# Optimization experiments

Hardware: AMD Instinct MI355X
Metric: run time of the kernel (lower is better)

The kernel has to match this reference:

```python
import jax, jax.numpy as jnp
import numpy as np

KSIZE = 16  # sliding window length (module ksize)


def setup_inputs() -> dict:
    key = jax.random.key(0)
    k0, k1, k2, k3, k4 = jax.random.split(key, 5)
    B, L, D, H = 16, 1024, 256, 256
    s = 1.0 / np.sqrt(H)  # torch RNN default init: U(-1/sqrt(H), 1/sqrt(H))
    x = jax.random.normal(k0, (B, L, D), dtype=jnp.float32)
    W_ih = jax.random.uniform(k1, (3 * H, D), jnp.float32, -s, s)  # [r|z|n] rows
    W_hh = jax.random.uniform(k2, (3 * H, H), jnp.float32, -s, s)
    b_ih = jax.random.uniform(k3, (3 * H,), jnp.float32, -s, s)
    b_hh = jax.random.uniform(k4, (3 * H,), jnp.float32, -s, s)
    return {"x": x, "W_ih": W_ih, "W_hh": W_hh, "b_ih": b_ih, "b_hh": b_hh}


def reference(x, W_ih, W_hh, b_ih, b_hh):
    # LocalRNN forward: for each position l, run a GRU over the window
    # x[l-K+1 : l+1] (zero left-padded) and emit the final hidden state.
    # Instead of materializing the [B, L, K, D] windowed copy (torch get_K),
    # we scan over the K window steps, slicing the padded input each step.
    B, L, D = x.shape
    H = W_hh.shape[1]
    K = KSIZE
    xpad = jnp.concatenate([jnp.zeros((B, K - 1, D), x.dtype), x], axis=1)  # [B, L+K-1, D]

    def step(h, t):
        xt = jax.lax.dynamic_slice_in_dim(xpad, t, L, axis=1)  # [B, L, D] = window step t for every position
        gi = jnp.einsum('bld,gd->blg', xt, W_ih) + b_ih          # [B, L, 3H]
        gh = jnp.einsum('blh,gh->blg', h, W_hh) + b_hh           # [B, L, 3H]
        i_r, i_z, i_n = jnp.split(gi, 3, axis=-1)
        h_r, h_z, h_n = jnp.split(gh, 3, axis=-1)
        r = jax.nn.sigmoid(i_r + h_r)
        z = jax.nn.sigmoid(i_z + h_z)
        n = jnp.tanh(i_n + r * h_n)
        h_new = (1.0 - z) * n + z * h  # torch GRU update
        return h_new, None

    h0 = jnp.zeros((B, L, H), x.dtype)
    h_final, _ = jax.lax.scan(step, h0, jnp.arange(K))
    return h_final  # [B, L, H] == h.view(batch, l, output_dim)
```

## Files before the change

### kernel.cpp

```cpp
#include <hip/hip_runtime.h>
#include <hip/hip_bf16.h>
#include <cstdint>


#define B_  16
#define L_  1024
#define D_  256
#define H_  256
#define K_  16
#define MT  32
#define NROW 47
#define HS  264
#define GRS 258
#define GNS 264
#define L2E 1.44269504f
#define NWR 196608

typedef __attribute__((ext_vector_type(8))) short  bf16x8;
typedef __attribute__((ext_vector_type(4))) float  floatx4;
typedef unsigned short ush;

#if __has_builtin(__builtin_amdgcn_exp2f)
#define fexp2(x) __builtin_amdgcn_exp2f(x)
#else
#define fexp2(x) exp2f(x)
#endif

__device__ __forceinline__ float bf2f(ush u) {
    union { unsigned int i; float f; } v; v.i = ((unsigned int)u) << 16; return v.f;
}
__device__ __forceinline__ ush f2bf(float f) {
    union { float f; unsigned int i; } v; v.f = f;
    unsigned int x = v.i;
    return (ush)((x + 0x7FFFu + ((x >> 16) & 1u)) >> 16);
}
__device__ __forceinline__ unsigned int pk2(float a, float b) {
    union { __hip_bfloat162 v; unsigned int u; } c;
    c.v = __float22bfloat162_rn(make_float2(a, b));
    return c.u;
}
__device__ __forceinline__ float rcpf(float x) { return __builtin_amdgcn_rcpf(x); }

#define NCHUNK 24576
__global__ __launch_bounds__(256) void wprep(const float* __restrict__ Wih,
                                             const float* __restrict__ Whh,
                                             ush* __restrict__ Wir,
                                             ush* __restrict__ Wr) {
    int idx = blockIdx.x * 256 + threadIdx.x;
    const float* src = (idx < NCHUNK) ? Whh : Wih;
    ush* dst         = (idx < NCHUNK) ? Wr  : Wir;
    int c = (idx < NCHUNK) ? idx : idx - NCHUNK;
    int srow = c >> 5, ch = c & 31;
    int gate = srow >> 8, rr = srow & 255;
    int w    = rr >> 5;
    int sloc = (rr >> 4) & 1;
    int l16  = rr & 15;
    int ks   = ch >> 2;
    int quad = ch & 3;
    int lane = quad * 16 + l16;
    int e0 = (((w * 6 + gate * 2 + sloc) * 8 + ks) << 9) + lane * 8;
    float scl = (gate < 2) ? -L2E : 2.f * L2E;
    const float* s = src + srow * 256 + ch * 8;
    float4 v0 = *(const float4*)(s);
    float4 v1 = *(const float4*)(s + 4);
    *(uint4*)(dst + e0) = make_uint4(pk2(v0.x * scl, v0.y * scl),
                                     pk2(v0.z * scl, v0.w * scl),
                                     pk2(v1.x * scl, v1.y * scl),
                                     pk2(v1.z * scl, v1.w * scl));
}

__global__ __launch_bounds__(512, 2) void rnn_fused(const float* __restrict__ x,
                                                    const ush* __restrict__ Wir,
                                                    const ush* __restrict__ Wr,
                                                    const float* __restrict__ bih,
                                                    const float* __restrict__ bhh,
                                                    float* __restrict__ out) {
    __shared__ __align__(16) ush xs[48 * HS];
    __shared__ unsigned int grz[NROW * GRS];
    __shared__ __align__(16) ush gn[NROW * GNS];
    __shared__ __align__(16) ush hl[2][MT * HS];

    int tid  = threadIdx.x;
    int wave = tid >> 6, lane = tid & 63;
    int l16  = lane & 15, quad = lane >> 4, quad4 = quad * 4;
    int p0   = blockIdx.x * MT;
    int bb   = p0 >> 10, lb = p0 & 1023;
    int base = wave * 32 + l16;

    {
        const float4* x4 = (const float4*)x;
        for (int idx = tid; idx < 48 * 64; idx += 512) {
            int j = idx >> 6, c = idx & 63;
            int tok = lb - 15 + j;
            float4 v = make_float4(0.f, 0.f, 0.f, 0.f);
            if (tok >= 0 && tok < L_) v = x4[(size_t)((bb << 10) + tok) * 64 + c];
            *(uint2*)(xs + j * HS + c * 4) = make_uint2(pk2(v.x, v.y), pk2(v.z, v.w));
        }
        for (int idx = tid; idx < MT * HS / 2; idx += 512)
            ((unsigned int*)(&hl[0][0]))[idx] = 0u;
    }
    __syncthreads();

    {
        floatx4 gacc[3][6];
#pragma unroll
        for (int sl = 0; sl < 2; sl++) {
            int cs = base + sl * 16;
            float ir = -L2E * (bih[cs] + bhh[cs]);
            float iz = -L2E * (bih[256 + cs] + bhh[256 + cs]);
            float in_ = 2.f * L2E * bih[512 + cs];
#pragma unroll
            for (int mt = 0; mt < 3; mt++) {
                gacc[mt][0 + sl] = (floatx4){ir, ir, ir, ir};
                gacc[mt][2 + sl] = (floatx4){iz, iz, iz, iz};
                gacc[mt][4 + sl] = (floatx4){in_, in_, in_, in_};
            }
        }
        const ush* wp = Wir + (size_t)wave * 24576 + lane * 8;
#pragma unroll
        for (int ks = 0; ks < 8; ks++) {
            bf16x8 bw[6];
#pragma unroll
            for (int n = 0; n < 6; n++)
                bw[n] = *(const bf16x8*)(wp + ((n * 8 + ks) << 9));
#pragma unroll
            for (int mt = 0; mt < 3; mt++) {
                bf16x8 af = *(const bf16x8*)(xs + (mt * 16 + l16) * HS + ks * 32 + quad * 8);
#pragma unroll
                for (int n = 0; n < 6; n++)
                    gacc[mt][n] = __builtin_amdgcn_mfma_f32_16x16x32_bf16(
                        af, bw[n], gacc[mt][n], 0, 0, 0);
            }
        }
#pragma unroll
        for (int mt = 0; mt < 3; mt++)
#pragma unroll
            for (int sl = 0; sl < 2; sl++) {
                int cs = base + sl * 16;
#pragma unroll
                for (int r = 0; r < 4; r++) {
                    int j = mt * 16 + quad4 + r;
                    if (j < NROW) {
                        grz[j * GRS + cs] = pk2(gacc[mt][0 + sl][r], gacc[mt][2 + sl][r]);
                        gn[j * GNS + cs]  = f2bf(gacc[mt][4 + sl][r]);
                    }
                }
            }
    }

    bf16x8 wf[6][8];
    {
        const ush* wp = Wr + (size_t)wave * 24576 + lane * 8;
#pragma unroll
        for (int n = 0; n < 6; n++)
#pragma unroll
            for (int ks = 0; ks < 8; ks++)
                wf[n][ks] = *(const bf16x8*)(wp + ((n * 8 + ks) << 9));
    }
    float bn0 = 2.f * L2E * bhh[512 + base];
    float bn1 = 2.f * L2E * bhh[512 + base + 16];
    float hreg[16];
#pragma unroll
    for (int q = 0; q < 16; q++) hreg[q] = 0.f;
    __syncthreads();

    for (int t = 0; t < K_; t++) {
        const ush* hc  = &hl[t & 1][0];
        ush*       hnx = &hl[(t + 1) & 1][0];
#pragma unroll
        for (int T = 0; T < 2; T++) {
#pragma unroll
            for (int sl = 0; sl < 2; sl++) {
                int col = base + sl * 16;
                int r0  = T * 16 + quad4 + t;
                unsigned int c0 = grz[(r0 + 0) * GRS + col];
                unsigned int c1 = grz[(r0 + 1) * GRS + col];
                unsigned int c2 = grz[(r0 + 2) * GRS + col];
                unsigned int c3 = grz[(r0 + 3) * GRS + col];
                float bn = sl ? bn1 : bn0;
                floatx4 a0 = (floatx4){0.f, 0.f, 0.f, 0.f};
                floatx4 a1 = (floatx4){0.f, 0.f, 0.f, 0.f};
                floatx4 a2 = (floatx4){bn, bn, bn, bn};
                const ush* ha = hc + (T * 16 + l16) * HS + quad * 8;
#pragma unroll
                for (int ks = 0; ks < 8; ks++) {
                    bf16x8 af = *(const bf16x8*)(ha + ks * 32);
                    a0 = __builtin_amdgcn_mfma_f32_16x16x32_bf16(af, wf[0 + sl][ks], a0, 0, 0, 0);
                    a1 = __builtin_amdgcn_mfma_f32_16x16x32_bf16(af, wf[2 + sl][ks], a1, 0, 0, 0);
                    a2 = __builtin_amdgcn_mfma_f32_16x16x32_bf16(af, wf[4 + sl][ks], a2, 0, 0, 0);
                }
                unsigned int cc[4] = {c0, c1, c2, c3};
                int hb = (T * 16 + quad4) * HS + col;
#pragma unroll
                for (int r = 0; r < 4; r++) {
                    float ar = a0[r] + __uint_as_float(cc[r] << 16);
                    float az = a1[r] + __uint_as_float(cc[r] & 0xffff0000u);
                    float rg = rcpf(1.f + fexp2(ar));
                    float zg = rcpf(1.f + fexp2(az));
                    float u  = bf2f(gn[(r0 + r) * GNS + col]) + rg * a2[r];
                    float ng = 1.f - 2.f * rcpf(fexp2(u) + 1.f);
                    int q = T * 8 + sl * 4 + r;
                    float hv = ng + zg * (hreg[q] - ng);
                    hreg[q] = hv;
                    hnx[hb + r * HS] = f2bf(hv);
                }
            }
        }
        __syncthreads();
    }
#pragma unroll
    for (int T = 0; T < 2; T++)
#pragma unroll
        for (int sl = 0; sl < 2; sl++)
#pragma unroll
            for (int r = 0; r < 4; r++) {
                int row = T * 16 + quad4 + r, col = base + sl * 16;
                out[(size_t)(p0 + row) * H_ + col] = hreg[T * 8 + sl * 4 + r];
            }
}

extern "C" void kernel_launch(void* const* d_in, const int* in_sizes, int n_in,
                              void* d_out, int out_size, void* d_ws, size_t ws_size,
                              hipStream_t stream) {
    const float* x    = (const float*)d_in[0];
    const float* W_ih = (const float*)d_in[1];
    const float* W_hh = (const float*)d_in[2];
    const float* b_ih = (const float*)d_in[3];
    const float* b_hh = (const float*)d_in[4];
    float* out = (float*)d_out;

    char* ws = (char*)d_ws;
    ush* Wir = (ush*)ws;
    ush* Wr  = (ush*)(ws + 393216);

    wprep<<<2 * NCHUNK / 256, 256, 0, stream>>>(W_ih, W_hh, Wir, Wr);
    rnn_fused<<<B_ * L_ / MT, 512, 0, stream>>>(x, Wir, Wr, b_ih, b_hh, out);
}
```

Baseline: 189.6 us.

## Halve per-block position tile to 16 and alias x staging with hidden buffers

Each block now handles 16 output positions instead of 32, so the input projection covers a 31-row halo instead of 47 and the grid doubles in size. The x staging buffer is reused as the double-buffered hidden-state buffer once the input projection finishes, which cuts LDS use and may allow more resident blocks. The cost is a larger halo fraction: redundant input-projection work per output rises from 47/32 to 31/16. Every block also reloads the full recurrent weight set into registers, so weight traffic per output doubles.

```diff
diff --git a/kernel.cpp b/kernel.cpp
--- a/kernel.cpp
+++ b/kernel.cpp
@@ -8,13 +8,12 @@
 #define D_  256
 #define H_  256
 #define K_  16
-#define MT  32
-#define NROW 47
+#define MT  16
+#define NROW 31
 #define HS  264
 #define GRS 258
 #define GNS 264
 #define L2E 1.44269504f
-#define NWR 196608
 
 typedef __attribute__((ext_vector_type(8))) short  bf16x8;
 typedef __attribute__((ext_vector_type(4))) float  floatx4;
@@ -75,10 +74,9 @@
                                                     const float* __restrict__ bih,
                                                     const float* __restrict__ bhh,
                                                     float* __restrict__ out) {
-    __shared__ __align__(16) ush xs[48 * HS];
+    __shared__ __align__(16) ush xh[2][MT * HS];
     __shared__ unsigned int grz[NROW * GRS];
     __shared__ __align__(16) ush gn[NROW * GNS];
-    __shared__ __align__(16) ush hl[2][MT * HS];
 
     int tid  = threadIdx.x;
     int wave = tid >> 6, lane = tid & 63;
@@ -87,22 +85,23 @@
     int bb   = p0 >> 10, lb = p0 & 1023;
     int base = wave * 32 + l16;
 
+    ush* xs = &xh[0][0];
+
     {
         const float4* x4 = (const float4*)x;
-        for (int idx = tid; idx < 48 * 64; idx += 512) {
+        for (int idx = tid; idx < 32 * 64; idx += 512) {
             int j = idx >> 6, c = idx & 63;
             int tok = lb - 15 + j;
             float4 v = make_float4(0.f, 0.f, 0.f, 0.f);
-            if (tok >= 0 && tok < L_) v = x4[(size_t)((bb << 10) + tok) * 64 + c];
+            if (j < NROW && tok >= 0 && tok < L_)
+                v = x4[(size_t)((bb << 10) + tok) * 64 + c];
             *(uint2*)(xs + j * HS + c * 4) = make_uint2(pk2(v.x, v.y), pk2(v.z, v.w));
         }
-        for (int idx = tid; idx < MT * HS / 2; idx += 512)
-            ((unsigned int*)(&hl[0][0]))[idx] = 0u;
     }
     __syncthreads();
 
     {
-        floatx4 gacc[3][6];
+        floatx4 gacc[2][6];
 #pragma unroll
         for (int sl = 0; sl < 2; sl++) {
             int cs = base + sl * 16;
@@ -110,7 +109,7 @@
             float iz = -L2E * (bih[256 + cs] + bhh[256 + cs]);
             float in_ = 2.f * L2E * bih[512 + cs];
 #pragma unroll
-            for (int mt = 0; mt < 3; mt++) {
+            for (int mt = 0; mt < 2; mt++) {
                 gacc[mt][0 + sl] = (floatx4){ir, ir, ir, ir};
                 gacc[mt][2 + sl] = (floatx4){iz, iz, iz, iz};
                 gacc[mt][4 + sl] = (floatx4){in_, in_, in_, in_};
@@ -124,7 +123,7 @@
             for (int n = 0; n < 6; n++)
                 bw[n] = *(const bf16x8*)(wp + ((n * 8 + ks) << 9));
 #pragma unroll
-            for (int mt = 0; mt < 3; mt++) {
+            for (int mt = 0; mt < 2; mt++) {
                 bf16x8 af = *(const bf16x8*)(xs + (mt * 16 + l16) * HS + ks * 32 + quad * 8);
 #pragma unroll
                 for (int n = 0; n < 6; n++)
@@ -133,7 +132,7 @@
             }
         }
 #pragma unroll
-        for (int mt = 0; mt < 3; mt++)
+        for (int mt = 0; mt < 2; mt++)
 #pragma unroll
             for (int sl = 0; sl < 2; sl++) {
                 int cs = base + sl * 16;
@@ -147,6 +146,10 @@
                 }
             }
     }
+    __syncthreads();
+
+    for (int idx = tid; idx < MT * HS / 2; idx += 512)
+        ((unsigned int*)(&xh[0][0]))[idx] = 0u;
 
     bf16x8 wf[6][8];
     {
@@ -159,64 +162,59 @@
     }
     float bn0 = 2.f * L2E * bhh[512 + base];
     float bn1 = 2.f * L2E * bhh[512 + base + 16];
-    float hreg[16];
-#pragma unroll
-    for (int q = 0; q < 16; q++) hreg[q] = 0.f;
+    float hreg[8];
+#pragma unroll
+    for (int q = 0; q < 8; q++) hreg[q] = 0.f;
     __syncthreads();
 
     for (int t = 0; t < K_; t++) {
-        const ush* hc  = &hl[t & 1][0];
-        ush*       hnx = &hl[(t + 1) & 1][0];
-#pragma unroll
-        for (int T = 0; T < 2; T++) {
-#pragma unroll
-            for (int sl = 0; sl < 2; sl++) {
-                int col = base + sl * 16;
-                int r0  = T * 16 + quad4 + t;
-                unsigned int c0 = grz[(r0 + 0) * GRS + col];
-                unsigned int c1 = grz[(r0 + 1) * GRS + col];
-                unsigned int c2 = grz[(r0 + 2) * GRS + col];
-                unsigned int c3 = grz[(r0 + 3) * GRS + col];
-                float bn = sl ? bn1 : bn0;
-                floatx4 a0 = (floatx4){0.f, 0.f, 0.f, 0.f};
-                floatx4 a1 = (floatx4){0.f, 0.f, 0.f, 0.f};
-                floatx4 a2 = (floatx4){bn, bn, bn, bn};
-                const ush* ha = hc + (T * 16 + l16) * HS + quad * 8;
-#pragma unroll
-                for (int ks = 0; ks < 8; ks++) {
-                    bf16x8 af = *(const bf16x8*)(ha + ks * 32);
-                    a0 = __builtin_amdgcn_mfma_f32_16x16x32_bf16(af, wf[0 + sl][ks], a0, 0, 0, 0);
-                    a1 = __builtin_amdgcn_mfma_f32_16x16x32_bf16(af, wf[2 + sl][ks], a1, 0, 0, 0);
-                    a2 = __builtin_amdgcn_mfma_f32_16x16x32_bf16(af, wf[4 + sl][ks], a2, 0, 0, 0);
-                }
-                unsigned int cc[4] = {c0, c1, c2, c3};
-                int hb = (T * 16 + quad4) * HS + col;
-#pragma unroll
-                for (int r = 0; r < 4; r++) {
-                    float ar = a0[r] + __uint_as_float(cc[r] << 16);
-                    float az = a1[r] + __uint_as_float(cc[r] & 0xffff0000u);
-                    float rg = rcpf(1.f + fexp2(ar));
-                    float zg = rcpf(1.f + fexp2(az));
-                    float u  = bf2f(gn[(r0 + r) * GNS + col]) + rg * a2[r];
-                    float ng = 1.f - 2.f * rcpf(fexp2(u) + 1.f);
-                    int q = T * 8 + sl * 4 + r;
-                    float hv = ng + zg * (hreg[q] - ng);
-                    hreg[q] = hv;
-                    hnx[hb + r * HS] = f2bf(hv);
-                }
+        const ush* hc  = &xh[t & 1][0];
+        ush*       hnx = &xh[(t + 1) & 1][0];
+#pragma unroll
+        for (int sl = 0; sl < 2; sl++) {
+            int col = base + sl * 16;
+            int r0  = quad4 + t;
+            unsigned int c0 = grz[(r0 + 0) * GRS + col];
+            unsigned int c1 = grz[(r0 + 1) * GRS + col];
+            unsigned int c2 = grz[(r0 + 2) * GRS + col];
+            unsigned int c3 = grz[(r0 + 3) * GRS + col];
+            float bn = sl ? bn1 : bn0;
+            floatx4 a0 = (floatx4){0.f, 0.f, 0.f, 0.f};
+            floatx4 a1 = (floatx4){0.f, 0.f, 0.f, 0.f};
+            floatx4 a2 = (floatx4){bn, bn, bn, bn};
+            const ush* ha = hc + l16 * HS + quad * 8;
+#pragma unroll
+            for (int ks = 0; ks < 8; ks++) {
+                bf16x8 af = *(const bf16x8*)(ha + ks * 32);
+                a0 = __builtin_amdgcn_mfma_f32_16x16x32_bf16(af, wf[0 + sl][ks], a0, 0, 0, 0);
+                a1 = __builtin_amdgcn_mfma_f32_16x16x32_bf16(af, wf[2 + sl][ks], a1, 0, 0, 0);
+                a2 = __builtin_amdgcn_mfma_f32_16x16x32_bf16(af, wf[4 + sl][ks], a2, 0, 0, 0);
+            }
+            unsigned int cc[4] = {c0, c1, c2, c3};
+            int hb = quad4 * HS + col;
+#pragma unroll
+            for (int r = 0; r < 4; r++) {
+                float ar = a0[r] + __uint_as_float(cc[r] << 16);
+                float az = a1[r] + __uint_as_float(cc[r] & 0xffff0000u);
+                float rg = rcpf(1.f + fexp2(ar));
+                float zg = rcpf(1.f + fexp2(az));
+                float u  = bf2f(gn[(r0 + r) * GNS + col]) + rg * a2[r];
+                float ng = 1.f - 2.f * rcpf(fexp2(u) + 1.f);
+                int q = sl * 4 + r;
+                float hv = ng + zg * (hreg[q] - ng);
+                hreg[q] = hv;
+                hnx[hb + r * HS] = f2bf(hv);
             }
         }
         __syncthreads();
     }
 #pragma unroll
-    for (int T = 0; T < 2; T++)
-#pragma unroll
-        for (int sl = 0; sl < 2; sl++)
-#pragma unroll
-            for (int r = 0; r < 4; r++) {
-                int row = T * 16 + quad4 + r, col = base + sl * 16;
-                out[(size_t)(p0 + row) * H_ + col] = hreg[T * 8 + sl * 4 + r];
-            }
+    for (int sl = 0; sl < 2; sl++)
+#pragma unroll
+        for (int r = 0; r < 4; r++) {
+            int row = quad4 + r, col = base + sl * 16;
+            out[(size_t)(p0 + row) * H_ + col] = hreg[sl * 4 + r];
+        }
 }
 
 extern "C" void kernel_launch(void* const* d_in, const int* in_sizes, int n_in,
```

New measurement: 218.1 us. 15.1% more time.
